# Performance work log

Measured on AMD Instinct MI355X. Metric: run time of the kernel, lower is better.

The kernel has to match this reference:

```python
import jax, jax.numpy as jnp
import numpy as np

N, X_DIM, Y_DIM, HID = 8192, 512, 2048 // 4, 2048
Y_DIM = 512

def setup_inputs() -> dict:
    key = jax.random.key(0)
    ks = jax.random.split(key, 10)
    def lin(k, fan_in, fan_out):
        lim = 1.0 / np.sqrt(fan_in)
        kw, kb = jax.random.split(k)
        W = jax.random.uniform(kw, (fan_in, fan_out), jnp.float32, -lim, lim)
        b = jax.random.uniform(kb, (fan_out,), jnp.float32, -lim, lim)
        return W, b
    mu_W1, mu_b1 = lin(ks[0], X_DIM, HID)
    mu_W2, mu_b2 = lin(ks[1], HID, Y_DIM)
    lv_W1, lv_b1 = lin(ks[2], X_DIM, HID)
    lv_W2, lv_b2 = lin(ks[3], HID, Y_DIM)
    return {
        "x_samples": jax.random.normal(ks[4], (N, X_DIM), jnp.float32),
        "y_samples": jax.random.normal(ks[5], (N, Y_DIM), jnp.float32),
        "mu_W1": mu_W1, "mu_b1": mu_b1, "mu_W2": mu_W2, "mu_b2": mu_b2,
        "lv_W1": lv_W1, "lv_b1": lv_b1, "lv_W2": lv_W2, "lv_b2": lv_b2,
    }

def reference(x_samples, y_samples, mu_W1, mu_b1, mu_W2, mu_b2, lv_W1, lv_b1, lv_W2, lv_b2):
    # MLP heads (GEMMs)
    mu = jax.nn.relu(x_samples @ mu_W1 + mu_b1) @ mu_W2 + mu_b2          # [N, D]
    logvar = jnp.tanh(jax.nn.relu(x_samples @ lv_W1 + lv_b1) @ lv_W2 + lv_b2)  # [N, D]
    w = 0.5 * jnp.exp(-logvar)                                           # 1/(2*exp(logvar))
    n = x_samples.shape[0]

    # positive: -mean_i sum_d (mu_id - y_id)^2 * w_id
    positive = -(((mu - y_samples) ** 2) * w).sum(axis=1).mean()

    # negative (exact decomposition of the [N,N,D] broadcast):
    # -(1/N^2) sum_{i,d} w_id * (N*mu_id^2 - 2*mu_id*Sy_d + Sy2_d)
    Sy = y_samples.sum(axis=0)          # [D]
    Sy2 = (y_samples ** 2).sum(axis=0)  # [D]
    negative = -(w * (n * mu ** 2 - 2.0 * mu * Sy + Sy2)).sum() / (n * n)

    return positive - negative
```

## Files before the change

### kernel.cpp

```cpp
#include <hip/hip_runtime.h>
#include <hip/hip_bf16.h>
#include <stdint.h>

#define NS   8192
#define XD   512
#define HD   2048
#define YD   512

typedef unsigned short u16;
using bf16x8 = __attribute__((ext_vector_type(8))) short;
using f32x4  = __attribute__((ext_vector_type(4))) float;

__device__ __forceinline__ float bf2f(u16 u) {
  union { uint32_t i; float f; } v; v.i = ((uint32_t)u) << 16; return v.f;
}
__device__ __forceinline__ u16 f2b(float f) {
  __hip_bfloat16 hb = __float2bfloat16(f);
  return *(const u16*)&hb;
}
__device__ __forceinline__ float ld_in(const void* p, int f32, size_t i) {
  return f32 ? ((const float*)p)[i] : bf2f(((const u16*)p)[i]);
}
#define GLDS(gp, lp) __builtin_amdgcn_global_load_lds( \
    (__attribute__((address_space(1))) void*)(gp),     \
    (__attribute__((address_space(3))) void*)(lp), 16, 0, 0)

__device__ __forceinline__ int probe_f32(const void* p, int n_u16, int* sflag) {
  if (threadIdx.x == 0) *sflag = 0;
  __syncthreads();
  const u16* q = (const u16*)p;
  int wild = 0;
  for (int i = threadIdx.x; i < n_u16; i += blockDim.x) {
    float v = bf2f(q[i]);
    if (!(fabsf(v) <= 1000.0f)) wild = 1;
  }
  if (wild) *sflag = 1;
  __syncthreads();
  int r = *sflag;
  __syncthreads();
  return r;
}

__global__ __launch_bounds__(256) void prep_all(
    const void* __restrict__ x,
    const void* w1m, const void* b1m, const void* w2m, const void* b2m,
    const void* w1l, const void* b1l, const void* w2l, const void* b2l,
    const void* __restrict__ y,
    u16* __restrict__ xb, float* __restrict__ biasv,
    u16* __restrict__ W1t, u16* __restrict__ W2tm, u16* __restrict__ W2tl,
    float* __restrict__ Sy, float* __restrict__ Sy2) {
  __shared__ u16 tile[64 * 72];
  __shared__ int sflag;
  const int b = blockIdx.x;
  const int tid = threadIdx.x;

  if (b < 2048) {
    if (!probe_f32(x, 1024, &sflag)) return;
    const size_t base = (size_t)b * 2048 + (size_t)tid * 8;
    alignas(16) u16 o[8];
    const float4* s = (const float4*)((const float*)x + base);
    float4 v0 = s[0], v1 = s[1];
    o[0]=f2b(v0.x); o[1]=f2b(v0.y); o[2]=f2b(v0.z); o[3]=f2b(v0.w);
    o[4]=f2b(v1.x); o[5]=f2b(v1.y); o[6]=f2b(v1.z); o[7]=f2b(v1.w);
    *(uint4*)(xb + base) = *(const uint4*)o;
  } else if (b == 2048) {
    const int f3 = probe_f32(b1m, 1024, &sflag);
    const int f5 = probe_f32(b2m, 512, &sflag);
    const int f7 = probe_f32(b1l, 1024, &sflag);
    const int f9 = probe_f32(b2l, 512, &sflag);
    for (int i = tid; i < 5120; i += 256) {
      float v;
      if (i < 2048)      v = ld_in(b1m, f3, i);
      else if (i < 4096) v = ld_in(b1l, f7, i - 2048);
      else if (i < 4608) v = ld_in(b2m, f5, i - 4096);
      else               v = ld_in(b2l, f9, i - 4608);
      biasv[i] = v;
    }
  } else if (b < 3073) {
    const int id = b - 2049, which = id >> 8, t = id & 255;
    const void* in; u16* out; int R, C;
    if (which == 0)      { in = w1m; out = W1t;                   R = XD; C = HD; }
    else if (which == 1) { in = w2m; out = W2tm;                  R = HD; C = YD; }
    else if (which == 2) { in = w1l; out = W1t + (size_t)HD * XD; R = XD; C = HD; }
    else                 { in = w2l; out = W2tl;                  R = HD; C = YD; }
    const int f = probe_f32(in, 1024, &sflag);
    const int nbx = C >> 6;
    const int c0 = (t % nbx) * 64, r0 = (t / nbx) * 64;
    const int r = tid >> 2, cc = (tid & 3) * 16;
    if (f) {
      const float4* s = (const float4*)((const float*)in + (size_t)(r0 + r) * C + c0 + cc);
#pragma unroll
      for (int k = 0; k < 4; ++k) {
        float4 v = s[k];
        tile[r * 72 + cc + k * 4 + 0] = f2b(v.x);
        tile[r * 72 + cc + k * 4 + 1] = f2b(v.y);
        tile[r * 72 + cc + k * 4 + 2] = f2b(v.z);
        tile[r * 72 + cc + k * 4 + 3] = f2b(v.w);
      }
    } else {
      const uint4* s = (const uint4*)((const u16*)in + (size_t)(r0 + r) * C + c0 + cc);
      *(uint4*)&tile[r * 72 + cc]     = s[0];
      *(uint4*)&tile[r * 72 + cc + 8] = s[1];
    }
    __syncthreads();
    const int i = tid >> 2, jc = (tid & 3) * 16;
    alignas(16) u16 o[16];
#pragma unroll
    for (int j = 0; j < 16; ++j) o[j] = tile[(jc + j) * 72 + i];
    uint4* dq = (uint4*)&out[(size_t)(c0 + i) * R + r0 + jc];
    dq[0] = ((const uint4*)o)[0];
    dq[1] = ((const uint4*)o)[1];
  } else {
    const int id2 = b - 3073;
    const int yf = probe_f32(y, 1024, &sflag);
    const int half = tid >> 7;
    const int c0 = (tid & 127) * 4;
    const int r0 = id2 * 128 + half * 64;
    float s0 = 0.f, s1 = 0.f, s2 = 0.f, s3 = 0.f;
    float q0 = 0.f, q1 = 0.f, q2 = 0.f, q3 = 0.f;
    for (int r = r0; r < r0 + 64; r += 4) {
#pragma unroll
      for (int rr = 0; rr < 4; ++rr) {
        float v0, v1, v2, v3;
        if (yf) {
          const float4 t4 = *(const float4*)((const float*)y + (size_t)(r + rr) * YD + c0);
          v0 = t4.x; v1 = t4.y; v2 = t4.z; v3 = t4.w;
        } else {
          const uint2 t2 = *(const uint2*)((const u16*)y + (size_t)(r + rr) * YD + c0);
          v0 = bf2f((u16)(t2.x & 0xffff)); v1 = bf2f((u16)(t2.x >> 16));
          v2 = bf2f((u16)(t2.y & 0xffff)); v3 = bf2f((u16)(t2.y >> 16));
        }
        s0 += v0; q0 += v0 * v0;  s1 += v1; q1 += v1 * v1;
        s2 += v2; q2 += v2 * v2;  s3 += v3; q3 += v3 * v3;
      }
    }
    atomicAdd(&Sy[c0],     s0);  atomicAdd(&Sy2[c0],     q0);
    atomicAdd(&Sy[c0 + 1], s1);  atomicAdd(&Sy2[c0 + 1], q1);
    atomicAdd(&Sy[c0 + 2], s2);  atomicAdd(&Sy2[c0 + 2], q2);
    atomicAdd(&Sy[c0 + 3], s3);  atomicAdd(&Sy2[c0 + 3], q3);
  }
}

#define SYNC_PRE do { \
  __builtin_amdgcn_sched_barrier(0); \
  __builtin_amdgcn_s_barrier(); \
  asm volatile("s_waitcnt lgkmcnt(0)" ::: "memory"); \
  __builtin_amdgcn_sched_barrier(0); \
  __builtin_amdgcn_s_setprio(1); } while (0)
#define SYNC_POST do { \
  __builtin_amdgcn_s_setprio(0); \
  __builtin_amdgcn_sched_barrier(0); \
  __builtin_amdgcn_s_barrier(); \
  __builtin_amdgcn_sched_barrier(0); } while (0)
#define VMCNT(N) asm volatile("s_waitcnt vmcnt(" #N ")" ::: "memory")

#define RD_A(MH, BUF) do { \
  const u16* ab_ = &lds[((BUF)*2 + wm) * 8192]; \
  _Pragma("unroll") for (int q_ = 0; q_ < 4; ++q_) \
    _Pragma("unroll") for (int ks_ = 0; ks_ < 2; ++ks_) \
      af[q_][ks_] = *(const bf16x8*)&ab_[((MH)*64 + q_*16 + c16)*64 + (((ks_*4+quad) ^ cswz) << 3)]; \
} while (0)

#define RD_B(NH, BUF) do { \
  const u16* bb_ = &lds[32768 + ((BUF)*2 + (wn>>1)) * 8192]; \
  _Pragma("unroll") for (int p_ = 0; p_ < 2; ++p_) \
    _Pragma("unroll") for (int ks_ = 0; ks_ < 2; ++ks_) \
      bf[(NH)*2+p_][ks_] = *(const bf16x8*)&bb_[((wn&1)*64 + ((NH)*2+p_)*16 + c16)*64 + (((ks_*4+quad) ^ cswz) << 3)]; \
} while (0)

#define MM(MH, NH) do { \
  _Pragma("unroll") for (int ks_ = 0; ks_ < 2; ++ks_) \
    _Pragma("unroll") for (int q_ = 0; q_ < 4; ++q_) \
      _Pragma("unroll") for (int p_ = 0; p_ < 2; ++p_) \
        acc[(MH)*4+q_][(NH)*2+p_] = __builtin_amdgcn_mfma_f32_16x16x32_bf16( \
            af[q_][ks_], bf[(NH)*2+p_][ks_], acc[(MH)*4+q_][(NH)*2+p_], 0, 0, 0); \
} while (0)

#define ST_A(KT, HALF) do { if ((KT) < 8) { \
  u16* lb_ = &lds[(((KT)&1)*2 + (HALF))*8192 + (wid << 9)]; \
  const u16* sp_ = Aptr + (size_t)(bm0 + (HALF)*128 + (wid<<3) + srow)*512 + ((KT)<<6) + scg; \
  GLDS(sp_, lb_); GLDS(sp_ + (size_t)64*512, lb_ + 4096); } } while (0)

#define ST_B(KT, HALF) do { if ((KT) < 8) { \
  u16* lb_ = &lds[32768 + (((KT)&1)*2 + (HALF))*8192 + (wid << 9)]; \
  const u16* sp_ = W1t + (size_t)(bn0 + (HALF)*128 + (wid<<3) + srow)*512 + ((KT)<<6) + scg; \
  GLDS(sp_, lb_); GLDS(sp_ + (size_t)64*512, lb_ + 4096); } } while (0)

__global__ __launch_bounds__(512, 2) void gemm1_kernel(
    const void* __restrict__ xraw, const u16* __restrict__ xb,
    const u16* __restrict__ W1t,
    const float* __restrict__ bias,
    u16* __restrict__ h_mu, u16* __restrict__ h_lv) {
  __shared__ alignas(16) u16 lds[65536];
  __shared__ int sflag;
  const int tid = threadIdx.x;

  const u16* Aptr = probe_f32(xraw, 1024, &sflag) ? xb : (const u16*)xraw;

  const int wid = tid >> 6, lane = tid & 63;
  const int wm = wid >> 2, wn = wid & 3;
  const int quad = lane >> 4, c16 = lane & 15, cswz = c16 & 7;
  const int srow = lane >> 3;
  const int scg  = ((lane & 7) ^ srow) << 3;

  const int id = blockIdx.x;
  const int xcd = id & 7, slot = id >> 3;
  const int bm0 = (xcd * 4 + (slot & 3)) * 256;
  const int bn0 = (slot >> 2) * 256;

  f32x4 acc[8][4] = {};
  bf16x8 af[4][2], bf[4][2];

  ST_B(0, 0); ST_B(0, 1); ST_A(0, 0); ST_A(0, 1);
  ST_B(1, 0); ST_B(1, 1);
  VMCNT(4);
  __builtin_amdgcn_s_barrier();
  __builtin_amdgcn_sched_barrier(0);

#pragma unroll
  for (int i = 0; i < 4; ++i) {
    const int ka = 2 * i, kb = ka + 1;
    const bool last = (i == 3);
    RD_A(0, 0); RD_B(0, 0); ST_A(kb, 0);
    SYNC_PRE; MM(0, 0); SYNC_POST;
    RD_B(1, 0); ST_A(kb, 1);
    SYNC_PRE; MM(0, 1); SYNC_POST;
    RD_A(1, 0); ST_B(ka + 2, 0);
    SYNC_PRE; MM(1, 0); SYNC_POST;
    ST_B(ka + 2, 1);
    SYNC_PRE; MM(1, 1);
    if (!last) { VMCNT(4); } else { VMCNT(0); }
    SYNC_POST;
    RD_A(0, 1); RD_B(0, 1); ST_A(ka + 2, 0);
    SYNC_PRE; MM(0, 0); SYNC_POST;
    RD_B(1, 1); ST_A(ka + 2, 1);
    SYNC_PRE; MM(0, 1); SYNC_POST;
    RD_A(1, 1); ST_B(kb + 2, 0);
    SYNC_PRE; MM(1, 0); SYNC_POST;
    ST_B(kb + 2, 1);
    SYNC_PRE; MM(1, 1);
    if (!last) { VMCNT(4); }
    SYNC_POST;
  }

  u16* myl = &lds[wid * 8192];
  const bool is_lv = bn0 >= HD;
  u16* dst = is_lv ? h_lv : h_mu;
  const int wncol = wn << 6;
  const int gc0 = (bn0 - (is_lv ? HD : 0)) + wncol;
  const int grow0 = bm0 + (wm << 7);
#pragma unroll
  for (int ni = 0; ni < 4; ++ni) {
    const float bv = bias[bn0 + wncol + ni * 16 + c16];
#pragma unroll
    for (int mi = 0; mi < 8; ++mi)
#pragma unroll
      for (int r = 0; r < 4; ++r) {
        const int row = mi * 16 + (quad << 2) + r;
        const int col = ni * 16 + c16;
        myl[row * 64 + ((((col >> 3) ^ (row & 7)) << 3) | (col & 7))] =
            f2b(fmaxf(acc[mi][ni][r] + bv, 0.f));
      }
  }
#pragma unroll
  for (int it = 0; it < 16; ++it) {
    const int row = (it << 3) + (lane >> 3);
    const int ch = lane & 7;
    const uint4 v = *(const uint4*)&myl[row * 64 + ((ch ^ (row & 7)) << 3)];
    *(uint4*)&dst[(size_t)(grow0 + row) * HD + gc0 + (ch << 3)] = v;
  }
}

#undef RD_A
#undef RD_B
#undef MM
#undef ST_A
#undef ST_B

#define RD_AF(RBASE, BUF) do { \
  _Pragma("unroll") for (int mi_ = 0; mi_ < 2; ++mi_) \
    _Pragma("unroll") for (int ks_ = 0; ks_ < 2; ++ks_) \
      afr[mi_][ks_] = *(const bf16x8*)&lds[(BUF)*32768 + (RBASE) + \
          (wm*32 + mi_*16 + c16)*64 + (((ks_*4+quad) ^ cswz) << 3)]; \
} while (0)

#define RD_BF4(RBASE, BUF) do { \
  _Pragma("unroll") for (int ni_ = 0; ni_ < 4; ++ni_) \
    _Pragma("unroll") for (int ks_ = 0; ks_ < 2; ++ks_) \
      bfr[ni_][ks_] = *(const bf16x8*)&lds[(BUF)*32768 + (RBASE) + \
          (wn*64 + ni_*16 + c16)*64 + (((ks_*4+quad) ^ cswz) << 3)]; \
} while (0)

#define MM16(accv) do { \
  _Pragma("unroll") for (int ks_ = 0; ks_ < 2; ++ks_) \
    _Pragma("unroll") for (int mi_ = 0; mi_ < 2; ++mi_) \
      _Pragma("unroll") for (int ni_ = 0; ni_ < 4; ++ni_) \
        accv[mi_][ni_] = __builtin_amdgcn_mfma_f32_16x16x32_bf16( \
            afr[mi_][ks_], bfr[ni_][ks_], accv[mi_][ni_], 0, 0, 0); \
} while (0)

#define ST_R(KT, SRC, RBASE) do { \
  u16* lb_ = &lds[(((KT)&1)*32768) + (RBASE) + (wid << 9)]; \
  const u16* sp_ = (SRC) + (size_t)(KT)*64; \
  GLDS(sp_, lb_); GLDS(sp_ + (size_t)64*2048, lb_ + 4096); \
} while (0)

#define RAm 0
#define RAl 8192
#define RBm 16384
#define RBl 24576

__global__ __launch_bounds__(512, 2) void gemm2_dual(
    const u16* __restrict__ hm, const u16* __restrict__ hl,
    const u16* __restrict__ W2m, const u16* __restrict__ W2l,
    const float* __restrict__ b2m, const float* __restrict__ b2l,
    const void* __restrict__ y,
    const float* __restrict__ Sy, const float* __restrict__ Sy2,
    double* __restrict__ gacc, unsigned* __restrict__ counter,
    float* __restrict__ out) {
  __shared__ alignas(16) u16 lds[65536];
  __shared__ double bs[8];
  __shared__ int sflag;

  const int yf = probe_f32(y, 1024, &sflag);

  const int tid = threadIdx.x, wid = tid >> 6, lane = tid & 63;
  const int wm = wid >> 1, wn = wid & 1;
  const int quad = lane >> 4, c16 = lane & 15, cswz = c16 & 7;
  const int srow = lane >> 3;
  const int scg  = ((lane & 7) ^ srow) << 3;

  const int id = blockIdx.x;
  const int xcd = id & 7, slot = id >> 3;
  const int bm0 = (xcd * 8 + (slot >> 2)) * 128;
  const int bn0 = (slot & 3) * 128;

  const u16* aM = hm  + (size_t)(bm0 + (wid << 3) + srow) * HD + scg;
  const u16* aL = hl  + (size_t)(bm0 + (wid << 3) + srow) * HD + scg;
  const u16* bM = W2m + (size_t)(bn0 + (wid << 3) + srow) * HD + scg;
  const u16* bL = W2l + (size_t)(bn0 + (wid << 3) + srow) * HD + scg;

  f32x4 am[2][4] = {}, al[2][4] = {};
  bf16x8 afr[2][2], bfr[4][2];

  ST_R(0, aM, RAm); ST_R(0, bM, RBm);
  ST_R(0, aL, RAl); ST_R(0, bL, RBl);
  ST_R(1, aM, RAm); ST_R(1, bM, RBm);
  VMCNT(8);
  __builtin_amdgcn_s_barrier();
  __builtin_amdgcn_sched_barrier(0);

#pragma unroll 1
  for (int i = 0; i < 15; ++i) {
    const int ka = 2 * i, kb = ka + 1;
    RD_AF(RAm, 0); RD_BF4(RBm, 0);
    ST_R(kb, aL, RAl); ST_R(kb, bL, RBl);
    SYNC_PRE; MM16(am); VMCNT(8); SYNC_POST;
    RD_AF(RAl, 0); RD_BF4(RBl, 0);
    ST_R(ka + 2, aM, RAm); ST_R(ka + 2, bM, RBm);
    SYNC_PRE; MM16(al); VMCNT(8); SYNC_POST;
    RD_AF(RAm, 1); RD_BF4(RBm, 1);
    ST_R(ka + 2, aL, RAl); ST_R(ka + 2, bL, RBl);
    SYNC_PRE; MM16(am); VMCNT(8); SYNC_POST;
    RD_AF(RAl, 1); RD_BF4(RBl, 1);
    ST_R(kb + 2, aM, RAm); ST_R(kb + 2, bM, RBm);
    SYNC_PRE; MM16(al); VMCNT(8); SYNC_POST;
  }
  RD_AF(RAm, 0); RD_BF4(RBm, 0);
  ST_R(31, aL, RAl); ST_R(31, bL, RBl);
  SYNC_PRE; MM16(am); VMCNT(8); SYNC_POST;
  RD_AF(RAl, 0); RD_BF4(RBl, 0);
  SYNC_PRE; MM16(al); VMCNT(4); SYNC_POST;
  RD_AF(RAm, 1); RD_BF4(RBm, 1);
  SYNC_PRE; MM16(am); VMCNT(0); SYNC_POST;
  RD_AF(RAl, 1); RD_BF4(RBl, 1);
  SYNC_PRE; MM16(al); SYNC_POST;

  const float invN = 1.0f / (float)NS;
  float s = 0.f;
#pragma unroll
  for (int ni = 0; ni < 4; ++ni) {
    const int gcol = bn0 + wn * 64 + ni * 16 + c16;
    const float bmv = b2m[gcol], blv = b2l[gcol];
    const float syv = Sy[gcol], sy2v = Sy2[gcol];
#pragma unroll
    for (int mi = 0; mi < 2; ++mi)
#pragma unroll
      for (int r = 0; r < 4; ++r) {
        const int grow = bm0 + wm * 32 + mi * 16 + quad * 4 + r;
        const float m   = am[mi][ni][r] + bmv;
        const float lvp = al[mi][ni][r] + blv;
        const float w   = 0.5f * expf(-tanhf(lvp));
        const float yv  = ld_in(y, yf, (size_t)grow * YD + gcol);
        s += w * (yv * yv - 2.f * m * yv + (2.f * m * syv - sy2v) * invN);
      }
  }
  for (int off = 32; off > 0; off >>= 1) s += __shfl_down(s, off);
  if (lane == 0) bs[wid] = (double)s;
  __syncthreads();
  if (tid == 0) {
    atomicAdd(gacc, bs[0] + bs[1] + bs[2] + bs[3] +
                    bs[4] + bs[5] + bs[6] + bs[7]);
    __threadfence();
    const unsigned old = atomicAdd(counter, 1u);
    if (old == gridDim.x - 1) {
      const double g = atomicAdd(gacc, 0.0);
      out[0] = (float)(-g / (double)NS);
    }
  }
}

extern "C" void kernel_launch(void* const* d_in, const int* in_sizes, int n_in,
                              void* d_out, int out_size, void* d_ws, size_t ws_size,
                              hipStream_t stream) {
  char* ws = (char*)d_ws;
  double*   gacc    = (double*)ws;
  unsigned* counter = (unsigned*)(ws + 8);
  float*    Sy      = (float*)(ws + 128);
  float*    Sy2     = (float*)(ws + 2176);
  float*    biasv   = (float*)(ws + 4224);
  u16* xb   = (u16*)(ws + 24704);
  u16* W1t  = xb + (size_t)NS * XD;
  u16* W2tm = W1t + (size_t)2 * HD * XD;
  u16* W2tl = W2tm + (size_t)YD * HD;
  u16* h_mu = W2tl + (size_t)YD * HD;
  u16* h_lv = h_mu + (size_t)NS * HD;

  hipMemsetAsync(d_ws, 0, 4224, stream);

  prep_all<<<2049 + 1024 + 64, 256, 0, stream>>>(
      d_in[0], d_in[2], d_in[3], d_in[4], d_in[5],
      d_in[6], d_in[7], d_in[8], d_in[9], d_in[1],
      xb, biasv, W1t, W2tm, W2tl, Sy, Sy2);

  const float* b1  = biasv;
  const float* b2m = biasv + 4096, *b2l = biasv + 4608;

  gemm1_kernel<<<(NS / 256) * ((2 * HD) / 256), 512, 0, stream>>>(
      d_in[0], xb, W1t, b1, h_mu, h_lv);

  gemm2_dual<<<(NS / 128) * (YD / 128), 512, 0, stream>>>(
      h_mu, h_lv, W2tm, W2tl, b2m, b2l, d_in[1], Sy, Sy2,
      gacc, counter, (float*)d_out);
}
```

Baseline: 220.2 us.

## Split waves across mu/logvar heads, load A fragments directly from global

Restructures the second-layer dual GEMM so half the waves compute the mu head and half the logvar head, each with a 64x64 tile per wave (4x4 MFMA accumulators). A fragments are now loaded straight from global memory into registers with inline asm, and only B (W2) tiles are staged through a 4-deep LDS ring. Mu results are then exchanged through LDS to the logvar waves for the epilogue. This cuts LDS traffic and barrier count per K-step, at the cost of more registers, uncoalesced direct global loads of A, and an epilogue where half the waves sit idle.

Result: slower. 258.7 us (+17.5%).

```diff
diff --git a/kernel.cpp b/kernel.cpp
--- a/kernel.cpp
+++ b/kernel.cpp
@@ -153,6 +153,7 @@
   __builtin_amdgcn_s_barrier(); \
   __builtin_amdgcn_sched_barrier(0); } while (0)
 #define VMCNT(N) asm volatile("s_waitcnt vmcnt(" #N ")" ::: "memory")
+#define SCB __builtin_amdgcn_sched_barrier(0)
 
 #define RD_A(MH, BUF) do { \
   const u16* ab_ = &lds[((BUF)*2 + wm) * 8192]; \
@@ -277,38 +278,59 @@
 #undef ST_A
 #undef ST_B
 
-#define RD_AF(RBASE, BUF) do { \
-  _Pragma("unroll") for (int mi_ = 0; mi_ < 2; ++mi_) \
-    _Pragma("unroll") for (int ks_ = 0; ks_ < 2; ++ks_) \
-      afr[mi_][ks_] = *(const bf16x8*)&lds[(BUF)*32768 + (RBASE) + \
-          (wm*32 + mi_*16 + c16)*64 + (((ks_*4+quad) ^ cswz) << 3)]; \
-} while (0)
-
-#define RD_BF4(RBASE, BUF) do { \
+#define LDA8(AF, T) do { \
+  const uint64_t o_ = (uint64_t)(T) * 128u; \
+  asm volatile("global_load_dwordx4 %0, %1, off" : "=v"(AF[0][0]) : "v"(aB[0] + o_)); \
+  asm volatile("global_load_dwordx4 %0, %1, off" : "=v"(AF[0][1]) : "v"(aB[1] + o_)); \
+  asm volatile("global_load_dwordx4 %0, %1, off" : "=v"(AF[1][0]) : "v"(aB[2] + o_)); \
+  asm volatile("global_load_dwordx4 %0, %1, off" : "=v"(AF[1][1]) : "v"(aB[3] + o_)); \
+  asm volatile("global_load_dwordx4 %0, %1, off" : "=v"(AF[2][0]) : "v"(aB[4] + o_)); \
+  asm volatile("global_load_dwordx4 %0, %1, off" : "=v"(AF[2][1]) : "v"(aB[5] + o_)); \
+  asm volatile("global_load_dwordx4 %0, %1, off" : "=v"(AF[3][0]) : "v"(aB[6] + o_)); \
+  asm volatile("global_load_dwordx4 %0, %1, off" : "=v"(AF[3][1]) : "v"(aB[7] + o_)); \
+} while (0)
+
+#define RD8(BF, BUFI) do { \
   _Pragma("unroll") for (int ni_ = 0; ni_ < 4; ++ni_) \
     _Pragma("unroll") for (int ks_ = 0; ks_ < 2; ++ks_) \
-      bfr[ni_][ks_] = *(const bf16x8*)&lds[(BUF)*32768 + (RBASE) + \
+      BF[ni_][ks_] = *(const bf16x8*)&lds[(BUFI)*16384 + rbase + \
           (wn*64 + ni_*16 + c16)*64 + (((ks_*4+quad) ^ cswz) << 3)]; \
 } while (0)
 
-#define MM16(accv) do { \
+#define MM32(AF, BF) do { \
   _Pragma("unroll") for (int ks_ = 0; ks_ < 2; ++ks_) \
-    _Pragma("unroll") for (int mi_ = 0; mi_ < 2; ++mi_) \
+    _Pragma("unroll") for (int mi_ = 0; mi_ < 4; ++mi_) \
       _Pragma("unroll") for (int ni_ = 0; ni_ < 4; ++ni_) \
-        accv[mi_][ni_] = __builtin_amdgcn_mfma_f32_16x16x32_bf16( \
-            afr[mi_][ks_], bfr[ni_][ks_], accv[mi_][ni_], 0, 0, 0); \
-} while (0)
-
-#define ST_R(KT, SRC, RBASE) do { \
-  u16* lb_ = &lds[(((KT)&1)*32768) + (RBASE) + (wid << 9)]; \
-  const u16* sp_ = (SRC) + (size_t)(KT)*64; \
-  GLDS(sp_, lb_); GLDS(sp_ + (size_t)64*2048, lb_ + 4096); \
-} while (0)
-
-#define RAm 0
-#define RAl 8192
-#define RBm 16384
-#define RBl 24576
+        acc[mi_][ni_] = __builtin_amdgcn_mfma_f32_16x16x32_bf16( \
+            AF[mi_][ks_], BF[ni_][ks_], acc[mi_][ni_], 0, 0, 0); \
+} while (0)
+
+#define ST3(KT, BUFI) do { \
+  u16* lbm_ = lds + (BUFI)*16384 + (wid << 9); \
+  const u16* spm_ = bMp + (size_t)(KT)*64; \
+  GLDS(spm_, lbm_); GLDS(spm_ + (size_t)64*HD, lbm_ + 4096); \
+  u16* lbl_ = lds + (BUFI)*16384 + 8192 + (wid << 9); \
+  const u16* spl_ = bLp + (size_t)(KT)*64; \
+  GLDS(spl_, lbl_); GLDS(spl_ + (size_t)64*HD, lbl_ + 4096); \
+} while (0)
+
+#define PH(T, AFc, AFn, BFc, BFn, RDB, STB) do { \
+  ST3((T) + 2, STB); \
+  SCB; \
+  LDA8(AFn, (T) + 1); \
+  SCB; \
+  VMCNT(20); \
+  __builtin_amdgcn_s_barrier(); \
+  SCB; \
+  RD8(BFn, RDB); \
+  SCB; \
+  VMCNT(12); \
+  SCB; \
+  __builtin_amdgcn_s_setprio(1); \
+  MM32(AFc, BFc); \
+  __builtin_amdgcn_s_setprio(0); \
+  SCB; \
+} while (0)
 
 __global__ __launch_bounds__(512, 2) void gemm2_dual(
     const u16* __restrict__ hm, const u16* __restrict__ hl,
@@ -325,75 +347,107 @@
   const int yf = probe_f32(y, 1024, &sflag);
 
   const int tid = threadIdx.x, wid = tid >> 6, lane = tid & 63;
-  const int wm = wid >> 1, wn = wid & 1;
+  const int wh = wid >> 2;
+  const int wm = (wid >> 1) & 1, wn = wid & 1;
   const int quad = lane >> 4, c16 = lane & 15, cswz = c16 & 7;
   const int srow = lane >> 3;
   const int scg  = ((lane & 7) ^ srow) << 3;
+  const int rbase = wh * 8192;
 
   const int id = blockIdx.x;
   const int xcd = id & 7, slot = id >> 3;
   const int bm0 = (xcd * 8 + (slot >> 2)) * 128;
   const int bn0 = (slot & 3) * 128;
 
-  const u16* aM = hm  + (size_t)(bm0 + (wid << 3) + srow) * HD + scg;
-  const u16* aL = hl  + (size_t)(bm0 + (wid << 3) + srow) * HD + scg;
-  const u16* bM = W2m + (size_t)(bn0 + (wid << 3) + srow) * HD + scg;
-  const u16* bL = W2l + (size_t)(bn0 + (wid << 3) + srow) * HD + scg;
-
-  f32x4 am[2][4] = {}, al[2][4] = {};
-  bf16x8 afr[2][2], bfr[4][2];
-
-  ST_R(0, aM, RAm); ST_R(0, bM, RBm);
-  ST_R(0, aL, RAl); ST_R(0, bL, RBl);
-  ST_R(1, aM, RAm); ST_R(1, bM, RBm);
+  const u16* bMp = W2m + (size_t)(bn0 + (wid << 3) + srow) * HD + scg;
+  const u16* bLp = W2l + (size_t)(bn0 + (wid << 3) + srow) * HD + scg;
+
+  const u16* hx = wh ? hl : hm;
+  uint64_t aB[8];
+#pragma unroll
+  for (int mi = 0; mi < 4; ++mi)
+#pragma unroll
+    for (int ks = 0; ks < 2; ++ks)
+      aB[mi * 2 + ks] = (uint64_t)(uintptr_t)(
+          hx + (size_t)(bm0 + wm * 64 + mi * 16 + c16) * HD + ks * 32 + quad * 8);
+
+  f32x4 acc[4][4] = {};
+  bf16x8 afA[4][2], afB[4][2], bfA[4][2], bfB[4][2];
+
+  ST3(0, 0); ST3(1, 1);
+  SCB;
+  LDA8(afA, 0);
+  SCB;
+  VMCNT(12);
+  __builtin_amdgcn_s_barrier();
+  SCB;
+  RD8(bfA, 0);
+  SCB;
+
+#pragma unroll 1
+  for (int i = 0; i < 28; i += 4) {
+    PH(i + 0, afA, afB, bfA, bfB, 1, 2);
+    PH(i + 1, afB, afA, bfB, bfA, 2, 3);
+    PH(i + 2, afA, afB, bfA, bfB, 3, 0);
+    PH(i + 3, afB, afA, bfB, bfA, 0, 1);
+  }
+  PH(28, afA, afB, bfA, bfB, 1, 2);
+  PH(29, afB, afA, bfB, bfA, 2, 3);
+  LDA8(afB, 31);
+  SCB;
+  VMCNT(16);
+  __builtin_amdgcn_s_barrier();
+  SCB;
+  RD8(bfB, 3);
+  SCB;
   VMCNT(8);
-  __builtin_amdgcn_s_barrier();
-  __builtin_amdgcn_sched_barrier(0);
-
-#pragma unroll 1
-  for (int i = 0; i < 15; ++i) {
-    const int ka = 2 * i, kb = ka + 1;
-    RD_AF(RAm, 0); RD_BF4(RBm, 0);
-    ST_R(kb, aL, RAl); ST_R(kb, bL, RBl);
-    SYNC_PRE; MM16(am); VMCNT(8); SYNC_POST;
-    RD_AF(RAl, 0); RD_BF4(RBl, 0);
-    ST_R(ka + 2, aM, RAm); ST_R(ka + 2, bM, RBm);
-    SYNC_PRE; MM16(al); VMCNT(8); SYNC_POST;
-    RD_AF(RAm, 1); RD_BF4(RBm, 1);
-    ST_R(ka + 2, aL, RAl); ST_R(ka + 2, bL, RBl);
-    SYNC_PRE; MM16(am); VMCNT(8); SYNC_POST;
-    RD_AF(RAl, 1); RD_BF4(RBl, 1);
-    ST_R(kb + 2, aM, RAm); ST_R(kb + 2, bM, RBm);
-    SYNC_PRE; MM16(al); VMCNT(8); SYNC_POST;
-  }
-  RD_AF(RAm, 0); RD_BF4(RBm, 0);
-  ST_R(31, aL, RAl); ST_R(31, bL, RBl);
-  SYNC_PRE; MM16(am); VMCNT(8); SYNC_POST;
-  RD_AF(RAl, 0); RD_BF4(RBl, 0);
-  SYNC_PRE; MM16(al); VMCNT(4); SYNC_POST;
-  RD_AF(RAm, 1); RD_BF4(RBm, 1);
-  SYNC_PRE; MM16(am); VMCNT(0); SYNC_POST;
-  RD_AF(RAl, 1); RD_BF4(RBl, 1);
-  SYNC_PRE; MM16(al); SYNC_POST;
-
+  SCB;
+  __builtin_amdgcn_s_setprio(1);
+  MM32(afA, bfA);
+  __builtin_amdgcn_s_setprio(0);
+  SCB;
+  VMCNT(0);
+  SCB;
+  __builtin_amdgcn_s_setprio(1);
+  MM32(afB, bfB);
+  __builtin_amdgcn_s_setprio(0);
+
+  __syncthreads();
+  float* ldsF = (float*)lds;
+  float* mur = ldsF + (wid & 3) * 4224;
+  if (wh == 0) {
+#pragma unroll
+    for (int ni = 0; ni < 4; ++ni) {
+      const float bmv = b2m[bn0 + wn * 64 + ni * 16 + c16];
+#pragma unroll
+      for (int mi = 0; mi < 4; ++mi)
+#pragma unroll
+        for (int r = 0; r < 4; ++r)
+          mur[(mi * 16 + quad * 4 + r) * 66 + ni * 16 + c16] =
+              acc[mi][ni][r] + bmv;
+    }
+  }
+  __syncthreads();
   const float invN = 1.0f / (float)NS;
   float s = 0.f;
-#pragma unroll
-  for (int ni = 0; ni < 4; ++ni) {
-    const int gcol = bn0 + wn * 64 + ni * 16 + c16;
-    const float bmv = b2m[gcol], blv = b2l[gcol];
-    const float syv = Sy[gcol], sy2v = Sy2[gcol];
-#pragma unroll
-    for (int mi = 0; mi < 2; ++mi)
-#pragma unroll
-      for (int r = 0; r < 4; ++r) {
-        const int grow = bm0 + wm * 32 + mi * 16 + quad * 4 + r;
-        const float m   = am[mi][ni][r] + bmv;
-        const float lvp = al[mi][ni][r] + blv;
-        const float w   = 0.5f * expf(-tanhf(lvp));
-        const float yv  = ld_in(y, yf, (size_t)grow * YD + gcol);
-        s += w * (yv * yv - 2.f * m * yv + (2.f * m * syv - sy2v) * invN);
-      }
+  if (wh == 1) {
+#pragma unroll
+    for (int ni = 0; ni < 4; ++ni) {
+      const int gcol = bn0 + wn * 64 + ni * 16 + c16;
+      const float blv = b2l[gcol];
+      const float syv = Sy[gcol], sy2v = Sy2[gcol];
+#pragma unroll
+      for (int mi = 0; mi < 4; ++mi)
+#pragma unroll
+        for (int r = 0; r < 4; ++r) {
+          const int grow = bm0 + wm * 64 + mi * 16 + quad * 4 + r;
+          const float m   = mur[(mi * 16 + quad * 4 + r) * 66 + ni * 16 + c16];
+          const float lvp = acc[mi][ni][r] + blv;
+          const float w   = 0.5f * expf(-tanhf(lvp));
+          const float yv  = ld_in(y, yf, (size_t)grow * YD + gcol);
+          s += w * (yv * yv - 2.f * m * yv + (2.f * m * syv - sy2v) * invN);
+        }
+    }
   }
   for (int off = 32; off > 0; off >>= 1) s += __shfl_down(s, off);
   if (lane == 0) bs[wid] = (double)s;
```
